# Kernel tuning notes

Measured on AMD Instinct MI355X. Metric: run time of the kernel, lower is better.

Reference implementation:

```python
import jax, jax.numpy as jnp
import numpy as np

N_QUBITS = 21
N_LAYERS = 3

# standard CNOT (control = first wire), reshaped for tensor contraction
_CNOT = np.array([[1, 0, 0, 0],
                  [0, 1, 0, 0],
                  [0, 0, 0, 1],
                  [0, 0, 1, 0]], dtype=np.complex64).reshape(2, 2, 2, 2)


def _rot(phi, theta, omega):
    """Rot(phi, theta, omega) = RZ(omega) RY(theta) RZ(phi), 2x2 complex64."""
    c = jnp.cos(theta * 0.5)
    s = jnp.sin(theta * 0.5)
    ep = jnp.exp(-0.5j * (phi + omega))   # e^{-i(phi+omega)/2}
    em = jnp.exp(0.5j * (phi - omega))    # e^{+i(phi-omega)/2}
    row0 = jnp.stack([ep * c, -em * s])
    row1 = jnp.stack([jnp.conj(em) * s, jnp.conj(ep) * c])
    return jnp.stack([row0, row1])


def _apply_1q(U, state, q):
    # contract gate with qubit axis q of state (shape (2,)*n)
    return jnp.moveaxis(jnp.tensordot(U, state, axes=((1,), (q,))), 0, q)


def _apply_cnot(state, q):
    # CNOT on adjacent qubits (q, q+1)
    out = jnp.tensordot(jnp.asarray(_CNOT), state, axes=((2, 3), (q, q + 1)))
    return jnp.moveaxis(out, (0, 1), (q, q + 1))


def _classifier(param, feat):
    n_layers, n_qubits = param.shape[0], param.shape[1]
    state = feat.astype(jnp.complex64).reshape((2,) * n_qubits)
    for i in range(n_layers):
        # layer of single-qubit Rot gates (== kron of per-qubit 2x2 unitaries)
        for j in range(n_qubits):
            U = _rot(param[i, j, 0], param[i, j, 1], param[i, j, 2])
            state = _apply_1q(U, state, j)
        # CNOT_layer: first pairs (0,1),(2,3),... then pairs (1,2),(3,4),...
        for q in range(0, n_qubits - 1, 2):
            state = _apply_cnot(state, q)
        for q in range(1, n_qubits - 1, 2):
            state = _apply_cnot(state, q)
    # sum over even flat indices == last qubit in |0>
    amp0 = state[..., 0]
    return jnp.sum(amp0.real ** 2 + amp0.imag ** 2)


def setup_inputs() -> dict:
    key = jax.random.key(0)
    k1, k2 = jax.random.split(key)
    feat = jax.random.normal(k1, (2 ** N_QUBITS,), dtype=jnp.float32)
    param = jax.random.uniform(k2, (N_LAYERS, N_QUBITS, 3),
                               dtype=jnp.float32,
                               minval=0.0, maxval=2.0 * np.pi)
    return {"feat": feat, "param": param}


def reference(feat, param):
    return _classifier(param, feat)
```

## Files before the change

kernel.cpp:

```cpp
#include <hip/hip_runtime.h>
#include <hip/hip_fp16.h>


typedef __attribute__((ext_vector_type(2))) float f2;

union H4 { int4 i4; __half2 h[4]; };
union H2 { int2 i2; __half2 h[2]; };

__device__ __forceinline__ f2 mkf2(float a, float b) { f2 r; r.x = a; r.y = b; return r; }

__device__ __forceinline__ unsigned SWZ(unsigned i) {
    return i ^ ((i >> 4) & 0xFu) ^ ((i >> 8) & 0xFu);
}
__device__ __forceinline__ unsigned f1(unsigned x, unsigned m) {
    return x ^ ((x >> 1) & m);
}
__device__ __forceinline__ unsigned f2fold(unsigned x, unsigned mA, unsigned mB) {
    unsigned t = x ^ ((x >> 1) & mA);
    return t ^ ((t >> 1) & mB);
}

__device__ __forceinline__ void crot(const f2 u00, const f2 u01,
                                     const f2 u10, const f2 u11,
                                     f2& a, f2& b) {
    const f2 sa = mkf2(-a.y, a.x);
    const f2 sb = mkf2(-b.y, b.x);
    f2 na = u00.x * a;
    na += u00.y * sa;
    na += u01.x * b;
    na += u01.y * sb;
    f2 nb = u10.x * a;
    nb += u10.y * sa;
    nb += u11.x * b;
    nb += u11.y * sb;
    a = na; b = nb;
}

__device__ __forceinline__ void apply4(f2 v[16], const f2* gU,
                                       int id0, int id1, int id2, int id3) {
    const int ids[4] = {id0, id1, id2, id3};
#pragma unroll
    for (int kk = 0; kk < 4; ++kk) {
        const int id = ids[kk];
        if (id < 0) continue;
        const f2 u00 = gU[4*id+0], u01 = gU[4*id+1];
        const f2 u10 = gU[4*id+2], u11 = gU[4*id+3];
#pragma unroll
        for (int x = 0; x < 16; ++x)
            if (!(x & (1 << kk)))
                crot(u00, u01, u10, u11, v[x], v[x | (1 << kk)]);
    }
}

__device__ __forceinline__ void prep_gates_lds(const float* __restrict__ param,
                                               f2* gU, unsigned tid) {
    if (tid < 63) {
        float phi = param[3*tid+0], th = param[3*tid+1], om = param[3*tid+2];
        float s, c;   __sincosf(0.5f*th, &s, &c);
        float sp, cp; __sincosf(-0.5f*(phi+om), &sp, &cp);
        float sm, cm; __sincosf( 0.5f*(phi-om), &sm, &cm);
        gU[4*tid+0] = mkf2( cp*c,  sp*c);
        gU[4*tid+1] = mkf2(-cm*s, -sm*s);
        gU[4*tid+2] = mkf2( cm*s, -sm*s);
        gU[4*tid+3] = mkf2( cp*c, -sp*c);
    }
}

__device__ __forceinline__ unsigned E1A (unsigned t, unsigned r){ return (t<<4)|r; }
__device__ __forceinline__ unsigned E2A (unsigned t, unsigned r){ return ((t>>4)<<8)|(r<<4)|(t&15u); }
__device__ __forceinline__ unsigned E3A (unsigned t, unsigned r){ return ((t>>8)<<12)|(r<<8)|(t&255u); }
__device__ __forceinline__ unsigned E4A (unsigned t, unsigned r){
    return (t&127u) | (((t>>7)&3u)<<10) | ((r&1u)<<7) | (((r>>1)&1u)<<8) | (((r>>2)&1u)<<9) | (((r>>3)&1u)<<12);
}
__device__ __forceinline__ unsigned E5A (unsigned t, unsigned r){
    return (t&31u) | (((t>>5)&7u)<<7) | (((t>>8)&1u)<<12) | ((r&1u)<<5) | (((r>>1)&1u)<<6) | (((r>>2)&1u)<<10) | (((r>>3)&1u)<<11);
}
__device__ __forceinline__ unsigned E6A (unsigned t, unsigned r){ return (t&1u) | (((t>>1)&255u)<<5) | (r<<1); }
__device__ __forceinline__ unsigned E7A (unsigned t, unsigned r){
    return ((t&63u)<<1) | (((t>>6)&7u)<<10) | (r&1u) | (((r>>1)&1u)<<7) | (((r>>2)&1u)<<8) | (((r>>3)&1u)<<9);
}
__device__ __forceinline__ unsigned E8A (unsigned t, unsigned r){ return (t&7u) | (((t>>3)&63u)<<7) | ((r&15u)<<3); }
__device__ __forceinline__ unsigned E11A(unsigned t, unsigned r){
    return (r&7u) | (((r>>3)&1u)<<8) | ((t&15u)<<9) | ((t>>4)<<3);
}
__device__ __forceinline__ unsigned E1B (unsigned t, unsigned r){ return (t&511u) | (r<<9); }
__device__ __forceinline__ unsigned E2B (unsigned t, unsigned r){ return (t&31u) | (((t>>5)&15u)<<9) | (r<<5); }
__device__ __forceinline__ unsigned E5B (unsigned t, unsigned r){
    return (t&15u) | (((t>>4)&31u)<<5) | ((r&1u)<<4) | (((r>>1)&1u)<<10) | (((r>>2)&1u)<<11) | (((r>>3)&1u)<<12);
}
__device__ __forceinline__ unsigned E6B (unsigned t, unsigned r){ return (t&63u) | (((t>>6)&7u)<<10) | (r<<6); }
__device__ __forceinline__ unsigned E7B (unsigned t, unsigned r){ return (t&3u) | (((t>>2)&127u)<<6) | (r<<2); }

#define PHASE(BUF, EW, ER) do { \
    _Pragma("unroll") for (int r = 0; r < 16; ++r) { unsigned e_ = (EW); BUF[SWZ(e_)] = v[r]; } \
    __syncthreads(); \
    _Pragma("unroll") for (int r = 0; r < 16; ++r) { unsigned e_ = (ER); v[r] = BUF[SWZ(e_)]; } \
    } while (0)

__global__ __launch_bounds__(512, 2) void sweepA(const float* __restrict__ feat,
                                                 const float* __restrict__ param,
                                                 __half2* __restrict__ zbuf,
                                                 float* __restrict__ out) {
    __shared__ f2 sh0[8192];
    __shared__ f2 sh1[8192];
    __shared__ f2 gU[252];
    const unsigned tid = threadIdx.x;
    const unsigned F = blockIdx.x;
    if (F == 0 && tid == 0) out[0] = 0.0f;

    float4 fraw[4];
    {
        const float4* fp = (const float4*)(feat + (((size_t)F) << 13) + (tid << 4));
#pragma unroll
        for (int c = 0; c < 4; ++c) fraw[c] = fp[c];
    }
    prep_gates_lds(param, gU, tid);

    f2 v[16];
#pragma unroll
    for (int c = 0; c < 4; ++c) {
        v[4*c+0] = mkf2(fraw[c].x, 0.f); v[4*c+1] = mkf2(fraw[c].y, 0.f);
        v[4*c+2] = mkf2(fraw[c].z, 0.f); v[4*c+3] = mkf2(fraw[c].w, 0.f);
    }
    __syncthreads();
    apply4(v, gU, 20, 19, 18, 17);
    PHASE(sh0, E1A(tid,r), E2A(tid,r));
    apply4(v, gU, 16, 15, 14, 13);
    PHASE(sh1, E2A(tid,r), E3A(tid,r));
    apply4(v, gU, 12, 11, 10, 9);
    PHASE(sh0, E3A(tid,r), f2fold(E4A(tid,r), 0x155u, 0x2AAu));
    apply4(v, gU, 34, 33, 32, 8);
    PHASE(sh1, E4A(tid,r), f2fold(E5A(tid,r), 0x400u, 0x800u));
    apply4(v, gU, 36, 35, 31, 30);
    PHASE(sh0, E5A(tid,r), f2fold(E6A(tid,r), 0x140u, 0x2A0u));
    apply4(v, gU, 40, 39, 38, 37);
    PHASE(sh1, E6A(tid,r), f2fold(E7A(tid,r), 0x014u, 0x00Au));
    apply4(v, gU, 41, 55, 54, 53);
    PHASE(sh0, E7A(tid,r), f1(E8A(tid,r), 0x081u));
    apply4(v, gU, 59, 58, 57, 56);
    PHASE(sh1, E8A(tid,r), f2fold(E11A(tid,r), 0x050u, 0x028u));
    apply4(v, gU, 62, 61, 60, -1);

    {
        int2* zb2 = (int2*)zbuf;
        const unsigned sbase = (tid & 15u) | (F << 4) | ((tid >> 4) << 15);
#pragma unroll
        for (unsigned g = 0; g < 8; ++g) {
            H2 y;
            y.h[0] = __float22half2_rn(make_float2(v[g].x,      v[g].y));
            y.h[1] = __float22half2_rn(make_float2(v[g | 8u].x, v[g | 8u].y));
            zb2[sbase | (g << 12)] = y.i2;
        }
    }
}

__global__ __launch_bounds__(512, 2) void sweepB(const __half2* __restrict__ zbuf,
                                                 const float* __restrict__ param,
                                                 float* __restrict__ out) {
    __shared__ f2 sh0[8192];
    __shared__ f2 sh1[8192];
    __shared__ f2 gU[252];
    __shared__ float wsum[8];
    const unsigned tid = threadIdx.x;
    const unsigned B = blockIdx.x * 2u;

    unsigned t0 = B ^ ((B >> 1) & 5u);
    const unsigned Bp = t0 ^ ((t0 >> 1) & 2u);
    H4 x[4];
    {
        const int4* src = (const int4*)(zbuf + (((size_t)Bp) << 13));
#pragma unroll
        for (unsigned c = 0; c < 4; ++c) x[c].i4 = src[c * 512 + tid];
    }
    prep_gates_lds(param, gU, tid);
#pragma unroll
    for (unsigned c = 0; c < 4; ++c) {
        unsigned e = (c << 11) | (tid << 2);
#pragma unroll
        for (unsigned k = 0; k < 4; ++k) {
            float2 t = __half22float2(x[c].h[k]);
            sh0[SWZ(e | k)] = mkf2(t.x, t.y);
        }
    }
    __syncthreads();

    f2 v[16];
#pragma unroll
    for (int r = 0; r < 16; ++r) v[r] = sh0[SWZ(E1B(tid,(unsigned)r))];
    apply4(v, gU, 3, 2, 1, 0);
    PHASE(sh1, E1B(tid,r), f1(E2B(tid,r), 0xA00u));
    apply4(v, gU, 7, 6, 5, 4);
    PHASE(sh0, E2B(tid,r), f2fold(E1B(tid,r), 0x550u, 0x0A0u));
    apply4(v, gU, 24, 23, 22, 21);
    PHASE(sh1, E1B(tid,r), f1(E2B(tid,r), 0xA00u));
    apply4(v, gU, 28, 27, 26, 25);
    PHASE(sh0, E2B(tid,r), f2fold(E5B(tid,r), 0x540u, 0x0A0u));
    apply4(v, gU, 29, 44, 43, 42);
    PHASE(sh1, E5B(tid,r), f2fold(E6B(tid,r), 0x014u, 0x008u));
    apply4(v, gU, 48, 47, 46, 45);
    PHASE(sh0, E6B(tid,r), E7B(tid,r));
    apply4(v, gU, 52, 51, 50, 49);
    float acc = 0.f;
#pragma unroll
    for (int r = 0; r < 16; ++r) acc += v[r].x*v[r].x + v[r].y*v[r].y;
    for (int off = 32; off; off >>= 1) acc += __shfl_down(acc, off);
    if ((tid & 63u) == 0) wsum[tid >> 6] = acc;
    __syncthreads();
    if (tid == 0) {
        float s = 0.f;
#pragma unroll
        for (int w = 0; w < 8; ++w) s += wsum[w];
        atomicAdd(out, s);
    }
}

extern "C" void kernel_launch(void* const* d_in, const int* in_sizes, int n_in,
                              void* d_out, int out_size, void* d_ws, size_t ws_size,
                              hipStream_t stream) {
    const float* feat  = (const float*)d_in[0];
    const float* param = (const float*)d_in[1];
    float* out = (float*)d_out;
    __half2* zbuf = (__half2*)d_ws;

    sweepA<<<256, 512, 0, stream>>>(feat, param, zbuf, out);
    sweepB<<<128, 512, 0, stream>>>(zbuf, param, out);
}
```

Measured before the change: 46.04 us.

## Split sweepB into smaller 128-thread blocks over 2048-amplitude sub-tiles

sweepB previously used 128 blocks of 512 threads, each holding an 8192-amplitude tile in LDS. It now uses 512 blocks of 128 threads that each process a 2048-amplitude sub-tile, which is possible because some qubit axes need no mixing in this stage. Each thread loads its 16 amplitudes straight from global memory into registers, skipping the initial LDS staging pass. The aim is to fill more CUs with less LDS per block. In exchange, the strided 4-byte global loads coalesce less well than the previous int4 loads, and the per-block gate prep and atomics are repeated across four times as many blocks.

```diff
diff --git a/kernel.cpp b/kernel.cpp
--- a/kernel.cpp
+++ b/kernel.cpp
@@ -83,13 +83,13 @@
 __device__ __forceinline__ unsigned E11A(unsigned t, unsigned r){
     return (r&7u) | (((r>>3)&1u)<<8) | ((t&15u)<<9) | ((t>>4)<<3);
 }
-__device__ __forceinline__ unsigned E1B (unsigned t, unsigned r){ return (t&511u) | (r<<9); }
-__device__ __forceinline__ unsigned E2B (unsigned t, unsigned r){ return (t&31u) | (((t>>5)&15u)<<9) | (r<<5); }
-__device__ __forceinline__ unsigned E5B (unsigned t, unsigned r){
-    return (t&15u) | (((t>>4)&31u)<<5) | ((r&1u)<<4) | (((r>>1)&1u)<<10) | (((r>>2)&1u)<<11) | (((r>>3)&1u)<<12);
-}
-__device__ __forceinline__ unsigned E6B (unsigned t, unsigned r){ return (t&63u) | (((t>>6)&7u)<<10) | (r<<6); }
-__device__ __forceinline__ unsigned E7B (unsigned t, unsigned r){ return (t&3u) | (((t>>2)&127u)<<6) | (r<<2); }
+__device__ __forceinline__ unsigned E1Bn(unsigned t, unsigned r){ return (t&127u) | (r<<7); }
+__device__ __forceinline__ unsigned E2Bn(unsigned t, unsigned r){ return (t&7u) | (r<<3) | ((t>>3)<<7); }
+__device__ __forceinline__ unsigned E5Bn(unsigned t, unsigned r){
+    return (t&3u) | ((r&1u)<<2) | (((t>>2)&31u)<<3) | (((r>>1)&1u)<<8) | (((r>>2)&1u)<<9) | (((r>>3)&1u)<<10);
+}
+__device__ __forceinline__ unsigned E6Bn(unsigned t, unsigned r){ return (t&15u) | (r<<4) | ((t>>4)<<8); }
+__device__ __forceinline__ unsigned E7Bn(unsigned t, unsigned r){ return (r&15u) | (t<<4); }
 
 #define PHASE(BUF, EW, ER) do { \
     _Pragma("unroll") for (int r = 0; r < 16; ++r) { unsigned e_ = (EW); BUF[SWZ(e_)] = v[r]; } \
@@ -154,51 +154,50 @@
     }
 }
 
-__global__ __launch_bounds__(512, 2) void sweepB(const __half2* __restrict__ zbuf,
+__global__ __launch_bounds__(128, 2) void sweepB(const __half2* __restrict__ zbuf,
                                                  const float* __restrict__ param,
                                                  float* __restrict__ out) {
-    __shared__ f2 sh0[8192];
-    __shared__ f2 sh1[8192];
+    __shared__ f2 sh0[2048];
+    __shared__ f2 sh1[2048];
     __shared__ f2 gU[252];
-    __shared__ float wsum[8];
+    __shared__ float wsum[2];
     const unsigned tid = threadIdx.x;
-    const unsigned B = blockIdx.x * 2u;
-
-    unsigned t0 = B ^ ((B >> 1) & 5u);
-    const unsigned Bp = t0 ^ ((t0 >> 1) & 2u);
-    H4 x[4];
+    const unsigned b = ((blockIdx.x & 7u) << 6) | (blockIdx.x >> 3);
+    const unsigned B8 = (b >> 2) << 1;
+    const unsigned t0 = B8 ^ ((B8 >> 1) & 5u);
+    const unsigned Bp8 = t0 ^ ((t0 >> 1) & 2u);
+    const unsigned zbase = (b & 1u) | (((b >> 1) & 1u) << 1) | (Bp8 << 13);
+
+    __half2 raw[16];
     {
-        const int4* src = (const int4*)(zbuf + (((size_t)Bp) << 13));
-#pragma unroll
-        for (unsigned c = 0; c < 4; ++c) x[c].i4 = src[c * 512 + tid];
+        const __half2* zp = zbuf + zbase;
+#pragma unroll
+        for (int r = 0; r < 16; ++r) {
+            unsigned ee = tid | ((unsigned)r << 7);
+            raw[r] = zp[(size_t)ee << 2];
+        }
     }
     prep_gates_lds(param, gU, tid);
-#pragma unroll
-    for (unsigned c = 0; c < 4; ++c) {
-        unsigned e = (c << 11) | (tid << 2);
-#pragma unroll
-        for (unsigned k = 0; k < 4; ++k) {
-            float2 t = __half22float2(x[c].h[k]);
-            sh0[SWZ(e | k)] = mkf2(t.x, t.y);
-        }
+
+    f2 v[16];
+#pragma unroll
+    for (int r = 0; r < 16; ++r) {
+        float2 t2 = __half22float2(raw[r]);
+        v[r] = mkf2(t2.x, t2.y);
     }
     __syncthreads();
-
-    f2 v[16];
-#pragma unroll
-    for (int r = 0; r < 16; ++r) v[r] = sh0[SWZ(E1B(tid,(unsigned)r))];
     apply4(v, gU, 3, 2, 1, 0);
-    PHASE(sh1, E1B(tid,r), f1(E2B(tid,r), 0xA00u));
+    PHASE(sh1, E1Bn(tid,r), f1(E2Bn(tid,r), 0x280u));
     apply4(v, gU, 7, 6, 5, 4);
-    PHASE(sh0, E2B(tid,r), f2fold(E1B(tid,r), 0x550u, 0x0A0u));
+    PHASE(sh0, E2Bn(tid,r), f2fold(E1Bn(tid,r), 0x154u, 0x028u));
     apply4(v, gU, 24, 23, 22, 21);
-    PHASE(sh1, E1B(tid,r), f1(E2B(tid,r), 0xA00u));
+    PHASE(sh1, E1Bn(tid,r), f1(E2Bn(tid,r), 0x280u));
     apply4(v, gU, 28, 27, 26, 25);
-    PHASE(sh0, E2B(tid,r), f2fold(E5B(tid,r), 0x540u, 0x0A0u));
+    PHASE(sh0, E2Bn(tid,r), f2fold(E5Bn(tid,r), 0x150u, 0x028u));
     apply4(v, gU, 29, 44, 43, 42);
-    PHASE(sh1, E5B(tid,r), f2fold(E6B(tid,r), 0x014u, 0x008u));
+    PHASE(sh1, E5Bn(tid,r), f2fold(E6Bn(tid,r), 0x005u, 0x002u));
     apply4(v, gU, 48, 47, 46, 45);
-    PHASE(sh0, E6B(tid,r), E7B(tid,r));
+    PHASE(sh0, E6Bn(tid,r), E7Bn(tid,r));
     apply4(v, gU, 52, 51, 50, 49);
     float acc = 0.f;
 #pragma unroll
@@ -206,12 +205,7 @@
     for (int off = 32; off; off >>= 1) acc += __shfl_down(acc, off);
     if ((tid & 63u) == 0) wsum[tid >> 6] = acc;
     __syncthreads();
-    if (tid == 0) {
-        float s = 0.f;
-#pragma unroll
-        for (int w = 0; w < 8; ++w) s += wsum[w];
-        atomicAdd(out, s);
-    }
+    if (tid == 0) atomicAdd(out, wsum[0] + wsum[1]);
 }
 
 extern "C" void kernel_launch(void* const* d_in, const int* in_sizes, int n_in,
@@ -223,5 +217,5 @@
     __half2* zbuf = (__half2*)d_ws;
 
     sweepA<<<256, 512, 0, stream>>>(feat, param, zbuf, out);
-    sweepB<<<128, 512, 0, stream>>>(zbuf, param, out);
-}
+    sweepB<<<512, 128, 0, stream>>>(zbuf, param, out);
+}
```

New measurement: 46.05 us. About the same (+0.0%).
